# Performance work log

Measured on AMD Instinct MI355X. Metric: run time of the kernel, lower is better.

Reference implementation:

```python
import jax, jax.numpy as jnp
import numpy as np

N_NODES = 100000
N_EDGES = 1600000
IN_FEATS = 128
HIDDEN = 128
OUT_FEATS = 40


def glorot(key, out_dim, in_dim):
    lim = np.sqrt(6.0 / (in_dim + out_dim)).astype(np.float32)
    return jax.random.uniform(key, (out_dim, in_dim), jnp.float32, -lim, lim)


def setup_inputs() -> dict:
    key = jax.random.key(0)
    ks = jax.random.split(key, 10)
    x = jax.random.normal(ks[0], (N_NODES, IN_FEATS), jnp.float32)
    edge_index = jax.random.randint(ks[1], (2, N_EDGES), 0, N_NODES, jnp.int32)
    return {
        "x": x,
        "edge_index": edge_index,
        # SAGEConv1: lin_l (on aggregated neighbors, with bias), lin_r (root, no bias)
        "W1_l": glorot(ks[2], HIDDEN, IN_FEATS),
        "b1": jnp.zeros((HIDDEN,), jnp.float32),
        "W1_r": glorot(ks[3], HIDDEN, IN_FEATS),
        # SAGEConv2
        "W2_l": glorot(ks[4], HIDDEN, HIDDEN),
        "b2": jnp.zeros((HIDDEN,), jnp.float32),
        "W2_r": glorot(ks[5], HIDDEN, HIDDEN),
        # classifier Linear
        "Wc": glorot(ks[6], OUT_FEATS, HIDDEN),
        "bc": jnp.zeros((OUT_FEATS,), jnp.float32),
    }


def _sage_conv(x, src, dst, W_l, b_l, W_r):
    # PyG SAGEConv with mean aggregation:
    # out = lin_l(mean_{j in N(i)} x_j) + lin_r(x_i)
    msg = x[src]                                   # [E, F] gather
    agg = jax.ops.segment_sum(msg, dst, num_segments=N_NODES)   # [N, F] scatter-add
    deg = jax.ops.segment_sum(jnp.ones((src.shape[0], 1), x.dtype), dst,
                              num_segments=N_NODES)             # [N, 1]
    agg = agg / jnp.maximum(deg, 1.0)
    return agg @ W_l.T + b_l + x @ W_r.T


def reference(x, edge_index, W1_l, b1, W1_r, W2_l, b2, W2_r, Wc, bc):
    src, dst = edge_index[0], edge_index[1]
    # dropout is identity in eval mode
    h = _sage_conv(x, src, dst, W1_l, b1, W1_r)
    h = jax.nn.relu(h)
    h = _sage_conv(h, src, dst, W2_l, b2, W2_r)
    embedding = h
    logits = embedding @ Wc.T + bc
    soft_label = jax.nn.softmax(logits, axis=1)
    hard_label = jnp.argmax(soft_label, axis=1)
    return logits, embedding, soft_label, hard_label
```

## Files before the change

### kernel.cpp

```cpp
#include <hip/hip_runtime.h>


#define FEATS 128
#define SCAN_CHUNK 4096

static __device__ __forceinline__ float4 ld4(const float* p) {
    return *reinterpret_cast<const float4*>(p);
}


__global__ __launch_bounds__(256)
void count_kernel(const int* __restrict__ dst, int* __restrict__ cnt, int E) {
    int i = blockIdx.x * 256 + threadIdx.x;
    if (i < E) atomicAdd(&cnt[dst[i]], 1);
}

__global__ __launch_bounds__(256)
void scan_partial(const int* __restrict__ cnt, int* __restrict__ part, int N) {
    __shared__ int red[256];
    const int base = blockIdx.x * SCAN_CHUNK;
    int sum = 0;
    for (int i = threadIdx.x; i < SCAN_CHUNK; i += 256) {
        int idx = base + i;
        sum += (idx < N) ? cnt[idx] : 0;
    }
    red[threadIdx.x] = sum;
    __syncthreads();
    for (int off = 128; off > 0; off >>= 1) {
        if (threadIdx.x < off) red[threadIdx.x] += red[threadIdx.x + off];
        __syncthreads();
    }
    if (threadIdx.x == 0) part[blockIdx.x] = red[0];
}

__global__ __launch_bounds__(1024)
void scan_part2(int* __restrict__ part, int nb, int* __restrict__ totalp) {
    __shared__ int s[1024];
    const int tid = threadIdx.x;
    s[tid] = (tid < nb) ? part[tid] : 0;
    __syncthreads();
    for (int off = 1; off < 1024; off <<= 1) {
        int t = (tid >= off) ? s[tid - off] : 0;
        __syncthreads();
        s[tid] += t;
        __syncthreads();
    }
    if (tid < nb) part[tid] = (tid == 0) ? 0 : s[tid - 1];
    if (tid == 0) *totalp = s[1023];
}

__global__ __launch_bounds__(256)
void scan_final(const int* __restrict__ cnt, const int* __restrict__ part,
                int* __restrict__ offs, int* __restrict__ cur, int N) {
    __shared__ int tsum[256];
    const int tid = threadIdx.x;
    const int myb = blockIdx.x * SCAN_CHUNK + tid * 16;
    int v[16];
    int s = 0;
    #pragma unroll
    for (int j = 0; j < 16; j++) {
        int idx = myb + j;
        int c = (idx < N) ? cnt[idx] : 0;
        v[j] = s; s += c;
    }
    tsum[tid] = s;
    __syncthreads();
    for (int off = 1; off < 256; off <<= 1) {
        int t = (tid >= off) ? tsum[tid - off] : 0;
        __syncthreads();
        tsum[tid] += t;
        __syncthreads();
    }
    const int base = part[blockIdx.x] + ((tid == 0) ? 0 : tsum[tid - 1]);
    #pragma unroll
    for (int j = 0; j < 16; j++) {
        int idx = myb + j;
        if (idx < N) { int o = base + v[j]; offs[idx] = o; cur[idx] = o; }
    }
}

__global__ __launch_bounds__(256)
void fill_kernel(const int* __restrict__ src, const int* __restrict__ dst,
                 int* __restrict__ cur, int* __restrict__ ssrc, int E) {
    int i = blockIdx.x * 256 + threadIdx.x;
    if (i < E) {
        int p = atomicAdd(&cur[dst[i]], 1);
        ssrc[p] = src[i];
    }
}

__global__ __launch_bounds__(256)
void agg_kernel(const float2* __restrict__ x2, const int* __restrict__ ssrc,
                const int* __restrict__ offs, float2* __restrict__ out2, int N) {
    const int g = blockIdx.x * 4 + (threadIdx.x >> 6);
    const int lane = threadIdx.x & 63;
    if (g >= N) return;
    const int beg = offs[g], end = offs[g + 1];
    float ax = 0.f, ay = 0.f;
    int e = beg;
    for (; e + 1 < end; e += 2) {
        int s0 = ssrc[e], s1 = ssrc[e + 1];
        float2 v0 = x2[(size_t)s0 * 64 + lane];
        float2 v1 = x2[(size_t)s1 * 64 + lane];
        ax += v0.x + v1.x; ay += v0.y + v1.y;
    }
    if (e < end) {
        int s0 = ssrc[e];
        float2 v0 = x2[(size_t)s0 * 64 + lane];
        ax += v0.x; ay += v0.y;
    }
    const int d = end - beg;
    const float inv = 1.0f / (float)(d > 1 ? d : 1);
    float2 o; o.x = ax * inv; o.y = ay * inv;
    out2[(size_t)g * 64 + lane] = o;
}

__global__ __launch_bounds__(256)
void sage_gemm(const float* __restrict__ A1, const float* __restrict__ A2,
               const float* __restrict__ Wl, const float* __restrict__ Wr,
               const float* __restrict__ bias, float* __restrict__ C,
               int M, int do_relu) {
    __shared__ float As[16][132];
    __shared__ float Bs[16][132];
    const int tid = threadIdx.x;
    const int tr = tid >> 4;
    const int tc = tid & 15;
    const int row0 = blockIdx.x * 128;
    const int lr = tid >> 2;
    const int lk = (tid & 3) << 2;
    const int bcol = tid >> 1;
    const int bkq = (tid & 1) << 3;

    float acc[8][8];
    #pragma unroll
    for (int m = 0; m < 8; m++)
        #pragma unroll
        for (int n = 0; n < 8; n++) acc[m][n] = 0.f;

    for (int kk = 0; kk < 16; kk++) {
        const float* Asrc = (kk < 8) ? A1 : A2;
        const float* Wsrc = (kk < 8) ? Wl : Wr;
        const int k0 = (kk & 7) << 4;

        #pragma unroll
        for (int h = 0; h < 2; h++) {
            const int r = lr + h * 64;
            const int gr = row0 + r;
            float4 av = make_float4(0.f, 0.f, 0.f, 0.f);
            if (gr < M) av = ld4(Asrc + (size_t)gr * FEATS + k0 + lk);
            As[lk + 0][r] = av.x; As[lk + 1][r] = av.y;
            As[lk + 2][r] = av.z; As[lk + 3][r] = av.w;
        }

        float4 b0 = ld4(Wsrc + (size_t)bcol * FEATS + k0 + bkq);
        float4 b1 = ld4(Wsrc + (size_t)bcol * FEATS + k0 + bkq + 4);
        Bs[bkq + 0][bcol] = b0.x; Bs[bkq + 1][bcol] = b0.y;
        Bs[bkq + 2][bcol] = b0.z; Bs[bkq + 3][bcol] = b0.w;
        Bs[bkq + 4][bcol] = b1.x; Bs[bkq + 5][bcol] = b1.y;
        Bs[bkq + 6][bcol] = b1.z; Bs[bkq + 7][bcol] = b1.w;
        __syncthreads();

        #pragma unroll
        for (int k = 0; k < 16; k++) {
            float4 a0 = *(const float4*)&As[k][tr * 8];
            float4 a1 = *(const float4*)&As[k][tr * 8 + 4];
            float4 b0v = *(const float4*)&Bs[k][tc * 8];
            float4 b1v = *(const float4*)&Bs[k][tc * 8 + 4];
            float am[8] = {a0.x, a0.y, a0.z, a0.w, a1.x, a1.y, a1.z, a1.w};
            float bn[8] = {b0v.x, b0v.y, b0v.z, b0v.w, b1v.x, b1v.y, b1v.z, b1v.w};
            #pragma unroll
            for (int m = 0; m < 8; m++)
                #pragma unroll
                for (int n = 0; n < 8; n++)
                    acc[m][n] += am[m] * bn[n];
        }
        __syncthreads();
    }

    float4 bv0 = ld4(bias + tc * 8);
    float4 bv1 = ld4(bias + tc * 8 + 4);
    float bb[8] = {bv0.x, bv0.y, bv0.z, bv0.w, bv1.x, bv1.y, bv1.z, bv1.w};
    #pragma unroll
    for (int m = 0; m < 8; m++) {
        const int r = row0 + tr * 8 + m;
        if (r < M) {
            float o[8];
            #pragma unroll
            for (int n = 0; n < 8; n++) {
                o[n] = acc[m][n] + bb[n];
                if (do_relu) o[n] = fmaxf(o[n], 0.f);
            }
            float* cp = C + (size_t)r * FEATS + tc * 8;
            *reinterpret_cast<float4*>(cp)     = make_float4(o[0], o[1], o[2], o[3]);
            *reinterpret_cast<float4*>(cp + 4) = make_float4(o[4], o[5], o[6], o[7]);
        }
    }
}

__global__ __launch_bounds__(256)
void classifier_kernel(const float* __restrict__ emb, const float* __restrict__ Wc,
                       const float* __restrict__ bc, float* __restrict__ logits,
                       float* __restrict__ soft, float* __restrict__ hard, int N) {
    __shared__ float Ws[40 * 128];
    __shared__ float bs[40];
    for (int i = threadIdx.x; i < 40 * 128; i += 256) Ws[i] = Wc[i];
    if (threadIdx.x < 40) bs[threadIdx.x] = bc[threadIdx.x];
    __syncthreads();
    const int row = blockIdx.x * 256 + threadIdx.x;
    if (row >= N) return;

    float acc[40];
    #pragma unroll
    for (int f = 0; f < 40; f++) acc[f] = 0.f;

    const float* erow = emb + (size_t)row * FEATS;
    for (int c = 0; c < 8; c++) {
        float4 r0 = ld4(erow + c * 16 + 0);
        float4 r1 = ld4(erow + c * 16 + 4);
        float4 r2 = ld4(erow + c * 16 + 8);
        float4 r3 = ld4(erow + c * 16 + 12);
        #pragma unroll
        for (int f = 0; f < 40; f++) {
            const float* w = &Ws[f * 128 + c * 16];
            float4 w0 = ld4(w), w1 = ld4(w + 4), w2 = ld4(w + 8), w3 = ld4(w + 12);
            acc[f] += r0.x * w0.x + r0.y * w0.y + r0.z * w0.z + r0.w * w0.w
                    + r1.x * w1.x + r1.y * w1.y + r1.z * w1.z + r1.w * w1.w
                    + r2.x * w2.x + r2.y * w2.y + r2.z * w2.z + r2.w * w2.w
                    + r3.x * w3.x + r3.y * w3.y + r3.z * w3.z + r3.w * w3.w;
        }
    }
    #pragma unroll
    for (int f = 0; f < 40; f++) acc[f] += bs[f];

    float m = acc[0]; int idx = 0;
    #pragma unroll
    for (int f = 1; f < 40; f++) { if (acc[f] > m) { m = acc[f]; idx = f; } }

    float* lrow = logits + (size_t)row * 40;
    #pragma unroll
    for (int f = 0; f < 40; f++) lrow[f] = acc[f];

    float sum = 0.f;
    #pragma unroll
    for (int f = 0; f < 40; f++) { acc[f] = __expf(acc[f] - m); sum += acc[f]; }
    const float inv = 1.0f / sum;
    float* srow = soft + (size_t)row * 40;
    #pragma unroll
    for (int f = 0; f < 40; f++) srow[f] = acc[f] * inv;
    hard[row] = (float)idx;
}


static inline size_t align16(size_t x) { return (x + 15) & ~(size_t)15; }

extern "C" void kernel_launch(void* const* d_in, const int* in_sizes, int n_in,
                              void* d_out, int out_size, void* d_ws, size_t ws_size,
                              hipStream_t stream) {
    const float* x   = (const float*)d_in[0];
    const int*   ei  = (const int*)d_in[1];
    const float* W1l = (const float*)d_in[2];
    const float* b1  = (const float*)d_in[3];
    const float* W1r = (const float*)d_in[4];
    const float* W2l = (const float*)d_in[5];
    const float* b2  = (const float*)d_in[6];
    const float* W2r = (const float*)d_in[7];
    const float* Wc  = (const float*)d_in[8];
    const float* bc  = (const float*)d_in[9];

    const int N = in_sizes[0] / FEATS;
    const int E = in_sizes[1] / 2;
    const int* src = ei;
    const int* dst = ei + E;
    const int nb = (N + SCAN_CHUNK - 1) / SCAN_CHUNK;

    char* ws = (char*)d_ws;
    size_t oCnt  = 0;
    size_t oOffs = oCnt  + align16((size_t)N * 4);
    size_t oCur  = oOffs + align16((size_t)(N + 1) * 4);
    size_t oPart = oCur  + align16((size_t)N * 4);
    size_t oSsrc = oPart + align16((size_t)nb * 4);
    size_t oAgg  = oSsrc + align16((size_t)E * 4);
    int*   cnt    = (int*)(ws + oCnt);
    int*   offs   = (int*)(ws + oOffs);
    int*   cur    = (int*)(ws + oCur);
    int*   part   = (int*)(ws + oPart);
    int*   ssrc   = (int*)(ws + oSsrc);
    float* aggbuf = (float*)(ws + oAgg);

    float* out    = (float*)d_out;
    float* logits = out;
    float* emb    = out + (size_t)N * 40;
    float* soft   = emb + (size_t)N * FEATS;
    float* hard   = soft + (size_t)N * 40;

    const int gridE = (E + 255) / 256;
    const int gridAgg = (N + 3) / 4;
    const int gridGemm = (N + 127) / 128;
    const int gridRow = (N + 255) / 256;

    hipMemsetAsync(cnt, 0, (size_t)N * 4, stream);
    count_kernel<<<gridE, 256, 0, stream>>>(dst, cnt, E);
    scan_partial<<<nb, 256, 0, stream>>>(cnt, part, N);
    scan_part2<<<1, 1024, 0, stream>>>(part, nb, offs + N);
    scan_final<<<nb, 256, 0, stream>>>(cnt, part, offs, cur, N);
    fill_kernel<<<gridE, 256, 0, stream>>>(src, dst, cur, ssrc, E);

    agg_kernel<<<gridAgg, 256, 0, stream>>>((const float2*)x, ssrc, offs, (float2*)aggbuf, N);
    sage_gemm<<<gridGemm, 256, 0, stream>>>(aggbuf, x, W1l, W1r, b1, emb, N, 1);

    agg_kernel<<<gridAgg, 256, 0, stream>>>((const float2*)emb, ssrc, offs, (float2*)aggbuf, N);
    sage_gemm<<<gridGemm, 256, 0, stream>>>(aggbuf, emb, W2l, W2r, b2, emb, N, 0);

    classifier_kernel<<<gridRow, 256, 0, stream>>>(emb, Wc, bc, logits, soft, hard, N);
}
```

Before: 829.8 us.

## Build CSR via two-level bucket sort with shared-memory atomics

Replaces the global-atomic count/fill CSR build with a radix-style two-pass bucket sort. Edges are first histogrammed per block into 512-node buckets in shared memory, scanned, and scattered as packed (local dst, src) words. A per-bucket kernel then does a local counting sort in LDS to produce offsets and sorted sources. This removes the heavily contended global atomics and random scattered writes, at the cost of an extra pass over the edges. The 17-bit src packing limits node count to 131072.

```diff
diff --git a/kernel.cpp b/kernel.cpp
--- a/kernel.cpp
+++ b/kernel.cpp
@@ -3,6 +3,10 @@
 
 #define FEATS 128
 #define SCAN_CHUNK 4096
+#define BSHIFT 9
+#define BSIZE  (1 << BSHIFT)
+#define MAXNB  256
+#define EPB    8192
 
 static __device__ __forceinline__ float4 ld4(const float* p) {
     return *reinterpret_cast<const float4*>(p);
@@ -10,9 +14,18 @@
 
 
 __global__ __launch_bounds__(256)
-void count_kernel(const int* __restrict__ dst, int* __restrict__ cnt, int E) {
-    int i = blockIdx.x * 256 + threadIdx.x;
-    if (i < E) atomicAdd(&cnt[dst[i]], 1);
+void hist_kernel(const int* __restrict__ dst, int* __restrict__ bhist,
+                 int E, int NB, int nblkA) {
+    __shared__ int hist[MAXNB];
+    const int tid = threadIdx.x, blk = blockIdx.x;
+    for (int t = tid; t < MAXNB; t += 256) hist[t] = 0;
+    __syncthreads();
+    const int e0 = blk * EPB;
+    const int e1 = min(E, e0 + EPB);
+    for (int i = e0 + tid; i < e1; i += 256)
+        atomicAdd(&hist[dst[i] >> BSHIFT], 1);
+    __syncthreads();
+    for (int t = tid; t < NB; t += 256) bhist[t * nblkA + blk] = hist[t];
 }
 
 __global__ __launch_bounds__(256)
@@ -50,8 +63,8 @@
 }
 
 __global__ __launch_bounds__(256)
-void scan_final(const int* __restrict__ cnt, const int* __restrict__ part,
-                int* __restrict__ offs, int* __restrict__ cur, int N) {
+void scan_out(const int* __restrict__ cnt, const int* __restrict__ part,
+              int* __restrict__ out, int Ntot) {
     __shared__ int tsum[256];
     const int tid = threadIdx.x;
     const int myb = blockIdx.x * SCAN_CHUNK + tid * 16;
@@ -60,7 +73,7 @@
     #pragma unroll
     for (int j = 0; j < 16; j++) {
         int idx = myb + j;
-        int c = (idx < N) ? cnt[idx] : 0;
+        int c = (idx < Ntot) ? cnt[idx] : 0;
         v[j] = s; s += c;
     }
     tsum[tid] = s;
@@ -75,17 +88,69 @@
     #pragma unroll
     for (int j = 0; j < 16; j++) {
         int idx = myb + j;
-        if (idx < N) { int o = base + v[j]; offs[idx] = o; cur[idx] = o; }
-    }
-}
-
-__global__ __launch_bounds__(256)
-void fill_kernel(const int* __restrict__ src, const int* __restrict__ dst,
-                 int* __restrict__ cur, int* __restrict__ ssrc, int E) {
-    int i = blockIdx.x * 256 + threadIdx.x;
-    if (i < E) {
-        int p = atomicAdd(&cur[dst[i]], 1);
-        ssrc[p] = src[i];
+        if (idx < Ntot) out[idx] = base + v[j];
+    }
+}
+
+__global__ __launch_bounds__(256)
+void scatter_kernel(const int* __restrict__ src, const int* __restrict__ dst,
+                    const int* __restrict__ scanT, int* __restrict__ packed,
+                    int E, int NB, int nblkA) {
+    __shared__ int cur[MAXNB];
+    const int tid = threadIdx.x, blk = blockIdx.x;
+    for (int t = tid; t < NB; t += 256) cur[t] = scanT[t * nblkA + blk];
+    __syncthreads();
+    const int e0 = blk * EPB;
+    const int e1 = min(E, e0 + EPB);
+    for (int i = e0 + tid; i < e1; i += 256) {
+        int d = dst[i], s = src[i];
+        int bkt = d >> BSHIFT;
+        int slot = atomicAdd(&cur[bkt], 1);
+        packed[slot] = ((d & (BSIZE - 1)) << 17) | s;
+    }
+}
+
+__global__ __launch_bounds__(256)
+void bucket_csr(const int* __restrict__ packed, const int* __restrict__ scanT,
+                int* __restrict__ offs, int* __restrict__ ssrc,
+                int N, int E, int NB, int nblkA) {
+    __shared__ int lcnt[BSIZE];
+    __shared__ int lofs[BSIZE];
+    __shared__ int s[256];
+    const int tid = threadIdx.x, b = blockIdx.x;
+    const int base_b = scanT[b * nblkA];
+    const int end_b = (b == NB - 1) ? E : scanT[(b + 1) * nblkA];
+    const int n0 = b << BSHIFT;
+    const int nn = min(BSIZE, N - n0);
+
+    lcnt[tid] = 0; lcnt[tid + 256] = 0;
+    __syncthreads();
+    for (int i = base_b + tid; i < end_b; i += 256)
+        atomicAdd(&lcnt[packed[i] >> 17], 1);
+    __syncthreads();
+
+    const int a0 = lcnt[2 * tid], a1 = lcnt[2 * tid + 1];
+    s[tid] = a0 + a1;
+    __syncthreads();
+    for (int off = 1; off < 256; off <<= 1) {
+        int t = (tid >= off) ? s[tid - off] : 0;
+        __syncthreads();
+        s[tid] += t;
+        __syncthreads();
+    }
+    const int ebase = (tid == 0) ? 0 : s[tid - 1];
+    lofs[2 * tid] = ebase;
+    lofs[2 * tid + 1] = ebase + a0;
+    __syncthreads();
+
+    for (int j = tid; j < nn; j += 256) offs[n0 + j] = base_b + lofs[j];
+    if (b == NB - 1 && tid == 0) offs[N] = E;
+    __syncthreads();
+
+    for (int i = base_b + tid; i < end_b; i += 256) {
+        int c = packed[i];
+        int slot = atomicAdd(&lofs[c >> 17], 1);
+        ssrc[base_b + slot] = c & 0x1FFFF;
     }
 }
 
@@ -271,21 +336,26 @@
     const int E = in_sizes[1] / 2;
     const int* src = ei;
     const int* dst = ei + E;
-    const int nb = (N + SCAN_CHUNK - 1) / SCAN_CHUNK;
+
+    const int NB    = (N + BSIZE - 1) >> BSHIFT;
+    const int nblkA = (E + EPB - 1) / EPB;
+    const int T     = NB * nblkA;
+    const int nb2   = (T + SCAN_CHUNK - 1) / SCAN_CHUNK;
 
     char* ws = (char*)d_ws;
-    size_t oCnt  = 0;
-    size_t oOffs = oCnt  + align16((size_t)N * 4);
-    size_t oCur  = oOffs + align16((size_t)(N + 1) * 4);
-    size_t oPart = oCur  + align16((size_t)N * 4);
-    size_t oSsrc = oPart + align16((size_t)nb * 4);
-    size_t oAgg  = oSsrc + align16((size_t)E * 4);
-    int*   cnt    = (int*)(ws + oCnt);
+    size_t oScanT = 0;
+    size_t oBhist = oScanT + align16((size_t)(T + 1) * 4);
+    size_t oPart  = oBhist + align16((size_t)T * 4);
+    size_t oOffs  = oPart  + align16((size_t)1024 * 4);
+    size_t oSsrc  = oOffs  + align16((size_t)(N + 1) * 4);
+    size_t oAgg   = oSsrc  + align16((size_t)E * 4);
+    int*   scanT  = (int*)(ws + oScanT);
+    int*   bhist  = (int*)(ws + oBhist);
+    int*   part   = (int*)(ws + oPart);
     int*   offs   = (int*)(ws + oOffs);
-    int*   cur    = (int*)(ws + oCur);
-    int*   part   = (int*)(ws + oPart);
     int*   ssrc   = (int*)(ws + oSsrc);
     float* aggbuf = (float*)(ws + oAgg);
+    int*   packed = (int*)(ws + oAgg);
 
     float* out    = (float*)d_out;
     float* logits = out;
@@ -293,17 +363,16 @@
     float* soft   = emb + (size_t)N * FEATS;
     float* hard   = soft + (size_t)N * 40;
 
-    const int gridE = (E + 255) / 256;
     const int gridAgg = (N + 3) / 4;
     const int gridGemm = (N + 127) / 128;
     const int gridRow = (N + 255) / 256;
 
-    hipMemsetAsync(cnt, 0, (size_t)N * 4, stream);
-    count_kernel<<<gridE, 256, 0, stream>>>(dst, cnt, E);
-    scan_partial<<<nb, 256, 0, stream>>>(cnt, part, N);
-    scan_part2<<<1, 1024, 0, stream>>>(part, nb, offs + N);
-    scan_final<<<nb, 256, 0, stream>>>(cnt, part, offs, cur, N);
-    fill_kernel<<<gridE, 256, 0, stream>>>(src, dst, cur, ssrc, E);
+    hist_kernel<<<nblkA, 256, 0, stream>>>(dst, bhist, E, NB, nblkA);
+    scan_partial<<<nb2, 256, 0, stream>>>(bhist, part, T);
+    scan_part2<<<1, 1024, 0, stream>>>(part, nb2, scanT + T);
+    scan_out<<<nb2, 256, 0, stream>>>(bhist, part, scanT, T);
+    scatter_kernel<<<nblkA, 256, 0, stream>>>(src, dst, scanT, packed, E, NB, nblkA);
+    bucket_csr<<<NB, 256, 0, stream>>>(packed, scanT, offs, ssrc, N, E, NB, nblkA);
 
     agg_kernel<<<gridAgg, 256, 0, stream>>>((const float2*)x, ssrc, offs, (float2*)aggbuf, N);
     sage_gemm<<<gridGemm, 256, 0, stream>>>(aggbuf, x, W1l, W1r, b1, emb, N, 1);
```

New measurement: 697.7 us. -15.9%, faster.
